# Optimization experiments

Measured on AMD Instinct MI355X. Metric: run time of the kernel, lower is better.

Reference implementation:

```python
import jax, jax.numpy as jnp
import numpy as np

EPS = 1e-8
EPS12 = 1e-12
TAU = 0.2
IOU_THRESHOLD = 0.5
NEG_INF = -1e9

N, C = 8192, 1024
HID, FGD, CLSD = 256, 64, 128


def setup_inputs() -> dict:
    key = jax.random.key(0)
    ks = jax.random.split(key, 16)
    roi_feats = jax.random.normal(ks[0], (N, C), dtype=jnp.float32)
    # labels in {-1 (ignore), 0 (bg), 1..20 (classes)}
    labels = jax.random.randint(ks[1], (N,), 0, 21, dtype=jnp.int64) - 1
    ious = jax.random.uniform(ks[2], (N,), dtype=jnp.float32)
    s = 0.02
    w1f = jax.random.normal(ks[3], (HID, C), dtype=jnp.float32) * s
    b1f = jnp.zeros((HID,), dtype=jnp.float32)
    w2f = jax.random.normal(ks[4], (FGD, HID), dtype=jnp.float32) * s
    b2f = jnp.zeros((FGD,), dtype=jnp.float32)
    w1c = jax.random.normal(ks[5], (HID, C), dtype=jnp.float32) * s
    b1c = jnp.zeros((HID,), dtype=jnp.float32)
    w2c = jax.random.normal(ks[6], (CLSD, HID), dtype=jnp.float32) * s
    b2c = jnp.zeros((CLSD,), dtype=jnp.float32)
    return {"roi_feats": roi_feats, "labels": labels, "ious": ious,
            "w1f": w1f, "b1f": b1f, "w2f": w2f, "b2f": b2f,
            "w1c": w1c, "b1c": b1c, "w2c": w2c, "b2c": b2c}


def _project_normalize(x, w1, b1, w2, b2):
    h = jax.nn.relu(x @ w1.T + b1)
    z = h @ w2.T + b2
    nrm = jnp.linalg.norm(z, axis=1, keepdims=True)  # F.normalize: z / max(||z||, eps)
    return z / jnp.maximum(nrm, EPS)


def _fg_bg_loss(z_fg, fg_mask, ignore_mask, iou_weight):
    n = z_fg.shape[0]
    anchor = fg_mask & ~ignore_mask
    eye = jnp.eye(n, dtype=bool)
    # pos_mask[i,j] = fg_mask[j] & ~ignore[j], self excluded
    pos = (fg_mask & ~ignore_mask)[None, :] & ~eye  # [N,N]
    sim = (z_fg @ z_fg.T) / TAU
    sim_exp = jnp.exp(sim) * (~eye).astype(sim.dtype)
    denom = sim_exp.sum(axis=1)  # [N]
    numer = jnp.sum(jnp.exp(sim) * pos.astype(sim.dtype), axis=1)  # [N]
    n_pos = pos.sum(axis=1)
    loss_i = -jnp.log((numer + EPS) / (denom + EPS))
    valid = anchor & (n_pos > 0)
    w = iou_weight
    num = jnp.sum(jnp.where(valid, loss_i * w, 0.0))
    den = jnp.sum(jnp.where(valid, w, 0.0)) + EPS
    return num / den


def _class_supcon_loss(z_cls, labels, fg_mask, ignore_mask, iou_weight):
    n = z_cls.shape[0]
    anchor = fg_mask & ~ignore_mask
    eye = jnp.eye(n, dtype=bool)
    valid_den = ~eye & ~ignore_mask[None, :]  # [N,N]
    # pos[i,j]: same label, j not ignored, labels[j] != 0, j != i, j valid
    pos = (labels[None, :] == labels[:, None]) & ~ignore_mask[None, :] & (labels[None, :] != 0)
    pos = pos & ~eye & valid_den
    sim = (z_cls @ z_cls.T) / TAU
    logits = jnp.where(valid_den, sim, NEG_INF)
    denom_log = jax.nn.logsumexp(logits, axis=1)  # [N]
    n_pos = pos.sum(axis=1)
    sum_pos = jnp.sum(jnp.where(pos, sim, 0.0), axis=1)
    n_pos_safe = jnp.maximum(n_pos, 1).astype(sim.dtype)
    loss_i = -(sum_pos - n_pos.astype(sim.dtype) * denom_log) / n_pos_safe
    valid = anchor & (n_pos > 0) & valid_den.any(axis=1)
    w = iou_weight
    num = jnp.sum(jnp.where(valid, loss_i * w, 0.0))
    den = jnp.sum(jnp.where(valid, w, 0.0)) + EPS12
    return num / den


def reference(roi_feats, labels, ious, w1f, b1f, w2f, b2f, w1c, b1c, w2c, b2c):
    z_fg = _project_normalize(roi_feats, w1f, b1f, w2f, b2f)
    z_cls = _project_normalize(roi_feats, w1c, b1c, w2c, b2c)
    ignore_mask = labels == -1
    bg_mask = (labels == 0) & ~ignore_mask
    fg_mask = (labels > 0) & ~ignore_mask
    iou_weight = jnp.where(ious > IOU_THRESHOLD, ious, 0.0)
    loss_fg_bg = _fg_bg_loss(z_fg, fg_mask, ignore_mask, iou_weight)
    loss_supcon = _class_supcon_loss(z_cls, labels, fg_mask, ignore_mask, iou_weight)
    # loss_weights = (1.0, 1.0); stacked as [loss_fg_bg, loss_supcon]
    return jnp.stack([loss_fg_bg * 1.0, loss_supcon * 1.0])
```

## Files before the change

### kernel.cpp

```cpp
#include <hip/hip_runtime.h>
#include <hip/hip_bf16.h>
#include <math.h>

#define N_ROI 8192
#define C_IN  1024
#define HIDD  256
#define FGD   64
#define CLSD  128
#define INV_TAU 5.0f
#define SCALE_LOG2E 7.2134752f
#define LN2F 0.69314718f

using frag_ab = __attribute__((ext_vector_type(8))) short;
using f32x16  = __attribute__((ext_vector_type(16))) float;

static __device__ __forceinline__ short f32_to_bf16_bits(float f) {
  unsigned u = __builtin_bit_cast(unsigned, f);
  u = (u + 0x7FFFu + ((u >> 16) & 1u)) >> 16;
  return (short)u;
}
static __device__ __forceinline__ float bf16_bits_to_f32(short b) {
  unsigned u = ((unsigned)(unsigned short)b) << 16;
  return __builtin_bit_cast(float, u);
}
static __device__ __forceinline__ float fast_exp2(float x) {
#if __has_builtin(__builtin_amdgcn_exp2f)
  return __builtin_amdgcn_exp2f(x);
#else
  return exp2f(x);
#endif
}
static __device__ __forceinline__ void async_copy16(const void* g, void* l) {
  __builtin_amdgcn_global_load_lds(
      (const __attribute__((address_space(1))) unsigned int*)g,
      (__attribute__((address_space(3))) unsigned int*)l, 16, 0, 0);
}

__global__ __launch_bounds__(256) void pack_zero_kernel(
    const float* __restrict__ w1f, const float* __restrict__ w1c,
    const float* __restrict__ w2f, const float* __restrict__ w2c,
    short* __restrict__ W1pf, short* __restrict__ W1pc,
    short* __restrict__ W2pf, short* __restrict__ W2pc,
    float* __restrict__ accum, int* __restrict__ cnt,
    float* __restrict__ Vc) {
  int b = blockIdx.x;
  if (b == 280) {
    int t = threadIdx.x;
    if (t < 8) accum[t] = 0.f;
    if (t < 24) cnt[t] = 0;
    for (int q = t; q < 2560; q += 256) Vc[q] = 0.f;
    return;
  }
  const float* src; short* dst; int Ksh; int b0;
  if (b < 128)      { src = w1f; dst = W1pf; Ksh = 10; b0 = 0; }
  else if (b < 256) { src = w1c; dst = W1pc; Ksh = 10; b0 = 128; }
  else if (b < 264) { src = w2f; dst = W2pf; Ksh = 8;  b0 = 256; }
  else              { src = w2c; dst = W2pc; Ksh = 8;  b0 = 264; }
  int K = 1 << Ksh;
  int f = (b - b0) * 256 + threadIdx.x;
  int r = f >> (Ksh - 3);
  int c0 = (f & ((K >> 3) - 1)) << 3;
  float4 v0 = *(const float4*)(src + (size_t)r * K + c0);
  float4 v1 = *(const float4*)(src + (size_t)r * K + c0 + 4);
  union { short s[8]; uint4 v; } o;
  o.s[0] = f32_to_bf16_bits(v0.x); o.s[1] = f32_to_bf16_bits(v0.y);
  o.s[2] = f32_to_bf16_bits(v0.z); o.s[3] = f32_to_bf16_bits(v0.w);
  o.s[4] = f32_to_bf16_bits(v1.x); o.s[5] = f32_to_bf16_bits(v1.y);
  o.s[6] = f32_to_bf16_bits(v1.z); o.s[7] = f32_to_bf16_bits(v1.w);
  ((uint4*)dst)[(size_t)((r >> 5) * (K >> 4) + (c0 >> 4)) * 64 +
                ((c0 >> 3) & 1) * 32 + (r & 31)] = o.v;
}

template<int D>
__device__ __forceinline__ void gemm2_from_lds(
    const short* __restrict__ T2,
    const short* __restrict__ W2p, const float* __restrict__ b2,
    short* __restrict__ Zr, float* __restrict__ tii,
    short* __restrict__ T, int gt) {
  int lane = threadIdx.x & 63;
  const frag_ab* Wv = (const frag_ab*)W2p;
  constexpr int NT = D / 32;
  frag_ab a[16];
  #pragma unroll
  for (int kc = 0; kc < 16; ++kc)
    a[kc] = *(const frag_ab*)&T2[(lane & 31) * 264 + kc * 16 + (lane >> 5) * 8];
  f32x16 acc[NT];
  #pragma unroll
  for (int j = 0; j < NT; ++j)
    #pragma unroll
    for (int q = 0; q < 16; ++q) acc[j][q] = 0.f;
  #pragma unroll
  for (int kc = 0; kc < 16; ++kc)
    #pragma unroll
    for (int j = 0; j < NT; ++j)
      acc[j] = __builtin_amdgcn_mfma_f32_32x32x16_bf16(a[kc], Wv[(j * 16 + kc) * 64 + lane], acc[j], 0, 0, 0);
  int c = lane & 31, h = lane >> 5;
  float bb[NT];
  #pragma unroll
  for (int j = 0; j < NT; ++j) bb[j] = b2[j * 32 + c];
  float s1[16];
  #pragma unroll
  for (int r = 0; r < 16; ++r) {
    s1[r] = 0.f;
    #pragma unroll
    for (int j = 0; j < NT; ++j) {
      float v = acc[j][r] + bb[j];
      s1[r] += v * v;
    }
  }
  #pragma unroll
  for (int r = 0; r < 16; ++r)
    #pragma unroll
    for (int m = 1; m < 32; m <<= 1) s1[r] += __shfl_xor(s1[r], m);
  float s2[16];
  #pragma unroll
  for (int r = 0; r < 16; ++r) s2[r] = 0.f;
  #pragma unroll
  for (int j = 0; j < NT; ++j) {
    int cl = j * 32 + c;
    #pragma unroll
    for (int g = 0; g < 4; ++g) {
      short q0, q1, q2, q3;
      #pragma unroll
      for (int e = 0; e < 4; ++e) {
        int r = g * 4 + e;
        float sc = 1.f / fmaxf(sqrtf(s1[r]), 1e-8f);
        short qb = f32_to_bf16_bits((acc[j][r] + bb[j]) * sc);
        float zf = bf16_bits_to_f32(qb);
        s2[r] += zf * zf;
        if (e == 0) q0 = qb; else if (e == 1) q1 = qb; else if (e == 2) q2 = qb; else q3 = qb;
      }
      *(short4*)&T[cl * 36 + 4 * h + 8 * g] = make_short4(q0, q1, q2, q3);
    }
  }
  #pragma unroll
  for (int r = 0; r < 16; ++r)
    #pragma unroll
    for (int m = 1; m < 32; m <<= 1) s2[r] += __shfl_xor(s2[r], m);
  if (c == 0) {
    #pragma unroll
    for (int r = 0; r < 16; ++r)
      tii[gt * 32 + (r & 3) + 8 * (r >> 2) + 4 * h] = s2[r];
  }
  uint4* Zv = (uint4*)Zr;
  #pragma unroll
  for (int k = 0; k < D / 16; ++k) {
    int c0 = (2 * k + h) * 8;
    union { short s[8]; uint4 u; } o;
    #pragma unroll
    for (int e = 0; e < 8; ++e) o.s[e] = T[(c0 + e) * 36 + c];
    Zv[(size_t)(gt * (D / 16) + k) * 64 + h * 32 + c] = o.u;
  }
}

__global__ __launch_bounds__(256) void fused_mlp_kernel(
    const float* __restrict__ X,
    const short* __restrict__ W1pf, const short* __restrict__ W1pc,
    const float* __restrict__ b1f, const float* __restrict__ b1c,
    const short* __restrict__ W2pf, const short* __restrict__ W2pc,
    const float* __restrict__ b2f, const float* __restrict__ b2c,
    short* __restrict__ Zrf, short* __restrict__ Zrc,
    float* __restrict__ tiif, float* __restrict__ tiic,
    const int* __restrict__ labels,
    float* __restrict__ Sfg, float* __restrict__ Pfg,
    float* __restrict__ Scls,
    float* __restrict__ pfv, float* __restrict__ nimv,
    int* __restrict__ cnt) {
  __shared__ short stageA[2][1024];
  __shared__ short T2[32 * 264];
  __shared__ short Tw[128 * 36];
  int tid = threadIdx.x, lane = tid & 63, wv = tid >> 6;
  int Mb = blockIdx.x, head = blockIdx.y;

  if (head == 0 && tid < 32) {
    int i = Mb * 32 + tid;
    Sfg[i] = 0.f; Pfg[i] = 0.f; Scls[i] = 0.f;
    int l = labels[i];
    pfv[i]  = (l > 0)  ? 1.f : 0.f;
    nimv[i] = (l != -1) ? 1.f : 0.f;
    int b = l + 1; if (b < 0) b = 0; if (b > 21) b = 21;
    atomicAdd(&cnt[b], 1);
  }

  const short* Wp = head ? W1pc : W1pf;
  const float* b1 = head ? b1c  : b1f;
  const uint4* Wv4 = (const uint4*)Wp;
  int arow = tid >> 3;
  int ac4  = tid & 7;
  const float* Xp = X + (size_t)(Mb * 32 + arow) * C_IN + ac4 * 4;
  int aslot = ((ac4 >> 2) * 64 + ((ac4 >> 1) & 1) * 32 + arow) * 8 + (ac4 & 1) * 4;

  float4 av[4];
  frag_ab breg[3][4];
  f32x16 acc[2];
  #pragma unroll
  for (int nt = 0; nt < 2; ++nt)
    #pragma unroll
    for (int q = 0; q < 16; ++q) acc[nt][q] = 0.f;

  auto loadA = [&](int c, int s) { av[s] = *(const float4*)(Xp + c * 32); };
  auto loadB = [&](int c, int s) {
    #pragma unroll
    for (int kci = 0; kci < 2; ++kci)
      #pragma unroll
      for (int nt = 0; nt < 2; ++nt)
        breg[s][kci * 2 + nt] =
            *(const frag_ab*)&Wv4[(size_t)((wv * 2 + nt) * 64 + c * 2 + kci) * 64 + lane];
  };
  auto storeA = [&](int buf, int s) {
    *(short4*)&stageA[buf][aslot] =
        make_short4(f32_to_bf16_bits(av[s].x), f32_to_bf16_bits(av[s].y),
                    f32_to_bf16_bits(av[s].z), f32_to_bf16_bits(av[s].w));
  };
  auto domfma = [&](int buf, int bank) {
    frag_ab a0 = *(const frag_ab*)&stageA[buf][(0 * 64 + lane) * 8];
    frag_ab a1 = *(const frag_ab*)&stageA[buf][(1 * 64 + lane) * 8];
    #pragma unroll
    for (int nt = 0; nt < 2; ++nt)
      acc[nt] = __builtin_amdgcn_mfma_f32_32x32x16_bf16(a0, breg[bank][nt], acc[nt], 0, 0, 0);
    #pragma unroll
    for (int nt = 0; nt < 2; ++nt)
      acc[nt] = __builtin_amdgcn_mfma_f32_32x32x16_bf16(a1, breg[bank][2 + nt], acc[nt], 0, 0, 0);
  };
  auto lds_barrier = [&]() {
    asm volatile("s_waitcnt lgkmcnt(0)" ::: "memory");
    __builtin_amdgcn_s_barrier();
    __builtin_amdgcn_sched_barrier(0);
  };

  loadA(0, 0); loadA(1, 1); loadA(2, 2); loadA(3, 3);
  loadB(0, 0); loadB(1, 1);
  storeA(0, 0);
  lds_barrier();

  #pragma unroll
  for (int c = 0; c < 32; ++c) {
    if (c + 2 < 32) loadB(c + 2, (c + 2) % 3);
    if (c + 4 < 32) loadA(c + 4, (c + 4) & 3);
    domfma(c & 1, c % 3);
    if (c + 1 < 32) {
      storeA((c + 1) & 1, (c + 1) & 3);
      lds_barrier();
    }
  }
  {
    int cl31 = lane & 31, h = lane >> 5;
    #pragma unroll
    for (int nt = 0; nt < 2; ++nt) {
      int gc = wv * 64 + nt * 32 + cl31;
      float bb = b1[gc];
      #pragma unroll
      for (int q = 0; q < 16; ++q) {
        int row = (q & 3) + 8 * (q >> 2) + 4 * h;
        float x = fmaxf(acc[nt][q] + bb, 0.f);
        T2[row * 264 + gc] = f32_to_bf16_bits(x);
      }
    }
  }
  __syncthreads();

  if (wv == 0) {
    if (head == 0)
      gemm2_from_lds<FGD>(T2, W2pf, b2f, Zrf, tiif, Tw, Mb);
    else
      gemm2_from_lds<CLSD>(T2, W2pc, b2c, Zrc, tiic, Tw, Mb);
  }
}

__global__ __launch_bounds__(128) void classsum_kernel(
    const short* __restrict__ Zrc, const int* __restrict__ labels,
    float* __restrict__ Vc) {
  __shared__ int lidx[512];
  __shared__ int lcnt;
  int c = blockIdx.x + 1;
  int d = threadIdx.x;
  int j0 = blockIdx.y * 512;
  if (d == 0) lcnt = 0;
  __syncthreads();
  #pragma unroll
  for (int u = 0; u < 4; ++u) {
    int row = j0 + u * 128 + d;
    if (labels[row] == c) {
      int k = atomicAdd(&lcnt, 1);
      lidx[k] = row;
    }
  }
  __syncthreads();
  int n = lcnt;
  int kc = d >> 4, h = (d >> 3) & 1, e = d & 7;
  float acc = 0.f;
  for (int k = 0; k < n; ++k) {
    int row = lidx[k];
    int jt = row >> 5, r = row & 31;
    acc += bf16_bits_to_f32(
        Zrc[((size_t)((jt * 8 + kc) * 64 + h * 32 + r)) * 8 + e]);
  }
  atomicAdd(&Vc[(c - 1) * 128 + d], acc);
}

template<int D, int MODE, int NJT>
__device__ __forceinline__ void loss_body(
    const short* __restrict__ Zr,
    const float* __restrict__ maskv,
    float* __restrict__ Sg, float* __restrict__ Pg,
    short* __restrict__ smem) {
  constexpr int KC = D / 16;
  constexpr int JP = 2;
  constexpr int NIT = NJT / JP;
  constexpr int BUFQ = JP * KC * 512;
  constexpr int LD = BUFQ / 4096;
  int tid = threadIdx.x, lane = tid & 63, wv = tid >> 6;
  int itile = (blockIdx.x >> 1) * 8 + wv;
  int jt0 = blockIdx.y * NJT;
  int jlane = lane & 31;
  const frag_ab* Zrv = (const frag_ab*)Zr;

  frag_ab a[KC];
  #pragma unroll
  for (int kc = 0; kc < KC; ++kc) {
    frag_ab t = Zrv[(itile * KC + kc) * 64 + lane];
    #pragma unroll
    for (int e = 0; e < 8; ++e)
      t[e] = f32_to_bf16_bits(bf16_bits_to_f32(t[e]) * SCALE_LOG2E);
    a[kc] = t;
  }
  __builtin_amdgcn_sched_barrier(0);
  asm volatile("s_waitcnt vmcnt(0)" ::: "memory");
  __builtin_amdgcn_sched_barrier(0);

  short* b0 = smem;
  short* b1 = smem + BUFQ;
  short* b2 = smem + 2 * BUFQ;
  float* maskf = (float*)(smem + 3 * BUFQ);

  async_copy16(maskv + jt0 * 32 + (size_t)(tid & 127) * 4,
               maskf + (wv & 1) * 256);

  auto STAGE = [&](short* dst, int it) {
    const short* src = Zr + (size_t)(jt0 + it * JP) * KC * 512;
    #pragma unroll
    for (int u = 0; u < LD; ++u)
      async_copy16(src + (size_t)(u * 512 + tid) * 8, dst + u * 4096 + wv * 512);
  };

  STAGE(b0, 0); STAGE(b1, 1);

  float Ssum[16] = {}, Psum[16] = {};

  #pragma unroll 1
  for (int t = 0; t < NIT; ++t) {
    if (t < NIT - 1) {
      if constexpr (LD == 1) asm volatile("s_waitcnt vmcnt(1)" ::: "memory");
      else                   asm volatile("s_waitcnt vmcnt(2)" ::: "memory");
    } else {
      asm volatile("s_waitcnt vmcnt(0)" ::: "memory");
    }
    __builtin_amdgcn_s_barrier();
    __builtin_amdgcn_sched_barrier(0);
    if (t + 2 < NIT) STAGE(b2, t + 2);

    float m0 = maskf[t * 64 + jlane];
    float m1 = maskf[t * 64 + 32 + jlane];
    f32x16 acc0, acc1;
    #pragma unroll
    for (int q = 0; q < 16; ++q) { acc0[q] = 0.f; acc1[q] = 0.f; }
    #pragma unroll
    for (int kc = 0; kc < KC; ++kc) {
      frag_ab bb0 = *(const frag_ab*)&b0[(kc * 64 + lane) * 8];
      frag_ab bb1 = *(const frag_ab*)&b0[((KC + kc) * 64 + lane) * 8];
      acc0 = __builtin_amdgcn_mfma_f32_32x32x16_bf16(a[kc], bb0, acc0, 0, 0, 0);
      acc1 = __builtin_amdgcn_mfma_f32_32x32x16_bf16(a[kc], bb1, acc1, 0, 0, 0);
    }
    #pragma unroll
    for (int rr = 0; rr < 16; ++rr) {
      float e0 = fast_exp2(acc0[rr]);
      float e1 = fast_exp2(acc1[rr]);
      if (MODE == 0) {
        Ssum[rr] += e0 + e1;
        Psum[rr] = fmaf(m0, e0, fmaf(m1, e1, Psum[rr]));
      } else {
        Ssum[rr] = fmaf(m1, e1, fmaf(m0, e0, Ssum[rr]));
      }
    }
    short* tmp = b0; b0 = b1; b1 = b2; b2 = tmp;
  }

  #pragma unroll
  for (int r = 0; r < 16; ++r) {
    float s = Ssum[r], p = Psum[r];
    #pragma unroll
    for (int m = 1; m < 32; m <<= 1) {
      s += __shfl_xor(s, m);
      if (MODE == 0) p += __shfl_xor(p, m);
    }
    if ((lane & 31) == 0) {
      int row = (r & 3) + 8 * (r >> 2) + 4 * (lane >> 5);
      atomicAdd(&Sg[itile * 32 + row], s);
      if (MODE == 0) atomicAdd(&Pg[itile * 32 + row], p);
    }
  }
}

__global__ __launch_bounds__(512, 2) void loss_kernel(
    const short* __restrict__ Zrf, const short* __restrict__ Zrc,
    const float* __restrict__ pfv, const float* __restrict__ nimv,
    float* __restrict__ Sfg, float* __restrict__ Pfg,
    float* __restrict__ Scls) {
  __shared__ short smem[3 * 8192 + 1024];
  if ((blockIdx.x & 1) == 0)
    loss_body<FGD, 0, 16>(Zrf, pfv, Sfg, Pfg, smem);
  else
    loss_body<CLSD, 1, 16>(Zrc, nimv, Scls, nullptr, smem);
}

__global__ __launch_bounds__(256) void finalize_kernel(
    const float* __restrict__ Sfg, const float* __restrict__ Pfg,
    const float* __restrict__ Scls,
    const short* __restrict__ Zrc, const float* __restrict__ Vc,
    const float* __restrict__ tiif, const float* __restrict__ tiic,
    const int* __restrict__ labels, const float* __restrict__ ious,
    int* __restrict__ cnt, float* __restrict__ accum, float* __restrict__ out) {
  int i = blockIdx.x * 256 + threadIdx.x;
  int l = labels[i];
  float iv = ious[i];
  float w = (iv > 0.5f) ? iv : 0.f;
  int cntP = 0;
  #pragma unroll
  for (int b = 2; b <= 21; ++b) cntP += cnt[b];
  int cntNI = N_ROI - cnt[0];
  bool Pi = (l > 0);
  float numF = 0.f, denF = 0.f, numC = 0.f, denC = 0.f;
  float eF = __expf(INV_TAU * tiif[i]);
  float Sf = Sfg[i] - eF;
  float Pf = Pfg[i] - (Pi ? eF : 0.f);
  int nposF = cntP - (Pi ? 1 : 0);
  if (Pi && nposF > 0) {
    float lossF = logf((Sf + 1e-8f) / (Pf + 1e-8f));
    numF = lossF * w; denF = w;
  }
  float tC = INV_TAU * tiic[i];
  float eC = __expf(tC);
  float Sc = Scls[i] - ((l != -1) ? eC : 0.f);
  float SPdot = 0.f;
  if (Pi) {
    const float* V = Vc + (size_t)(l - 1) * 128;
    int jt = i >> 5, r = i & 31;
    #pragma unroll
    for (int kc = 0; kc < 8; ++kc)
      #pragma unroll
      for (int h = 0; h < 2; ++h) {
        frag_ab z = *(const frag_ab*)&Zrc[((size_t)((jt * 8 + kc) * 64 + h * 32 + r)) * 8];
        #pragma unroll
        for (int e = 0; e < 8; ++e)
          SPdot += bf16_bits_to_f32(z[e]) * V[kc * 16 + h * 8 + e];
      }
  }
  float SP = SPdot * INV_TAU - (Pi ? tC : 0.f);
  int nposC = Pi ? (cnt[l + 1] - 1) : 0;
  bool anyv = (cntNI - ((l != -1) ? 1 : 0)) > 0;
  if (Pi && nposC > 0 && anyv) {
    float lse = logf(Sc);
    float lossC = -(SP - (float)nposC * lse) / fmaxf((float)nposC, 1.f);
    numC = lossC * w; denC = w;
  }
  float v0 = numF, v1 = denF, v2 = numC, v3 = denC;
  #pragma unroll
  for (int m = 1; m < 64; m <<= 1) {
    v0 += __shfl_xor(v0, m); v1 += __shfl_xor(v1, m);
    v2 += __shfl_xor(v2, m); v3 += __shfl_xor(v3, m);
  }
  __shared__ float red[4][4];
  int lane = threadIdx.x & 63, wid = threadIdx.x >> 6;
  if (lane == 0) { red[wid][0]=v0; red[wid][1]=v1; red[wid][2]=v2; red[wid][3]=v3; }
  __syncthreads();
  if (threadIdx.x == 0) {
    float s0=0,s1=0,s2=0,s3=0;
    for (int q = 0; q < 4; ++q) { s0+=red[q][0]; s1+=red[q][1]; s2+=red[q][2]; s3+=red[q][3]; }
    atomicAdd(&accum[0], s0); atomicAdd(&accum[1], s1);
    atomicAdd(&accum[2], s2); atomicAdd(&accum[3], s3);
    __threadfence();
    int t = atomicAdd(&cnt[22], 1);
    if (t == 31) {
      __threadfence();
      out[0] = accum[0] / (accum[1] + 1e-8f);
      out[1] = accum[2] / (accum[3] + 1e-12f);
    }
  }
}

extern "C" void kernel_launch(void* const* d_in, const int* in_sizes, int n_in,
                              void* d_out, int out_size, void* d_ws, size_t ws_size,
                              hipStream_t stream) {
  const float* X    = (const float*)d_in[0];
  const int*  labels= (const int*)d_in[1];
  const float* ious = (const float*)d_in[2];
  const float* w1f  = (const float*)d_in[3];
  const float* b1f  = (const float*)d_in[4];
  const float* w2f  = (const float*)d_in[5];
  const float* b2f  = (const float*)d_in[6];
  const float* w1c  = (const float*)d_in[7];
  const float* b1c  = (const float*)d_in[8];
  const float* w2c  = (const float*)d_in[9];
  const float* b2c  = (const float*)d_in[10];
  float* out = (float*)d_out;

  char* w = (char*)d_ws;
  short* W1pf = (short*)w;            w += 524288;
  short* W1pc = (short*)w;            w += 524288;
  short* W2pf = (short*)w;            w += 32768;
  short* W2pc = (short*)w;            w += 65536;
  short* Zrf  = (short*)w;            w += 1048576;
  short* Zrc  = (short*)w;            w += 2097152;
  float* Sfg  = (float*)w;            w += 32768;
  float* Pfg  = (float*)w;            w += 32768;
  float* Scls = (float*)w;            w += 32768;
  float* SPc  = (float*)w;            w += 32768;
  float* tiif = (float*)w;            w += 32768;
  float* tiic = (float*)w;            w += 32768;
  float* pfv  = (float*)w;            w += 32768;
  float* nimv = (float*)w;            w += 32768;
  float* ljmv = (float*)w;            w += 32768;
  float* accum= (float*)w;            w += 32;
  int*   cnt  = (int*)w;              w += 96;
  float* Vc   = (float*)w;            w += 10240;
  (void)SPc; (void)ljmv;

  pack_zero_kernel<<<281, 256, 0, stream>>>(w1f, w1c, w2f, w2c,
                                            W1pf, W1pc, W2pf, W2pc, accum, cnt, Vc);

  fused_mlp_kernel<<<dim3(256, 2), 256, 0, stream>>>(X, W1pf, W1pc, b1f, b1c,
                                            W2pf, W2pc, b2f, b2c,
                                            Zrf, Zrc, tiif, tiic,
                                            labels, Sfg, Pfg, Scls,
                                            pfv, nimv, cnt);

  classsum_kernel<<<dim3(20, 16), 128, 0, stream>>>(Zrc, labels, Vc);

  loss_kernel<<<dim3(64, 16), 512, 0, stream>>>(Zrf, Zrc, pfv, nimv,
                                                Sfg, Pfg, Scls);

  finalize_kernel<<<N_ROI/256, 256, 0, stream>>>(Sfg, Pfg, Scls, Zrc, Vc,
                                                 tiif, tiic,
                                                 labels, ious, cnt, accum, out);
}
```

Baseline: 184.3 us.

## Pre-pack X to bf16 MFMA layout and stream it via async LDS loads

```diff
diff --git a/kernel.cpp b/kernel.cpp
--- a/kernel.cpp
+++ b/kernel.cpp
@@ -37,10 +37,12 @@
 }
 
 __global__ __launch_bounds__(256) void pack_zero_kernel(
+    const float* __restrict__ X,
     const float* __restrict__ w1f, const float* __restrict__ w1c,
     const float* __restrict__ w2f, const float* __restrict__ w2c,
     short* __restrict__ W1pf, short* __restrict__ W1pc,
     short* __restrict__ W2pf, short* __restrict__ W2pc,
+    short* __restrict__ Xp16,
     float* __restrict__ accum, int* __restrict__ cnt,
     float* __restrict__ Vc) {
   int b = blockIdx.x;
@@ -49,6 +51,25 @@
     if (t < 8) accum[t] = 0.f;
     if (t < 24) cnt[t] = 0;
     for (int q = t; q < 2560; q += 256) Vc[q] = 0.f;
+    return;
+  }
+  if (b >= 281) {
+    int b2 = b - 281;
+    int Mb = b2 >> 4, cpair = b2 & 15;
+    int tid = threadIdx.x;
+    int c = cpair * 2 + (tid >> 7);
+    int tt = tid & 127;
+    int lane = tt & 63, kh = tt >> 6;
+    int row = lane & 31, hi = lane >> 5;
+    const float* src = X + (size_t)(Mb * 32 + row) * C_IN + c * 32 + kh * 16 + hi * 8;
+    float4 v0 = *(const float4*)src;
+    float4 v1 = *(const float4*)(src + 4);
+    union { short s[8]; uint4 v; } o;
+    o.s[0] = f32_to_bf16_bits(v0.x); o.s[1] = f32_to_bf16_bits(v0.y);
+    o.s[2] = f32_to_bf16_bits(v0.z); o.s[3] = f32_to_bf16_bits(v0.w);
+    o.s[4] = f32_to_bf16_bits(v1.x); o.s[5] = f32_to_bf16_bits(v1.y);
+    o.s[6] = f32_to_bf16_bits(v1.z); o.s[7] = f32_to_bf16_bits(v1.w);
+    *(uint4*)&Xp16[((size_t)(Mb * 32 + c)) * 1024 + (size_t)tt * 8] = o.v;
     return;
   }
   const float* src; short* dst; int Ksh; int b0;
@@ -154,7 +175,7 @@
 }
 
 __global__ __launch_bounds__(256) void fused_mlp_kernel(
-    const float* __restrict__ X,
+    const short* __restrict__ Xp16,
     const short* __restrict__ W1pf, const short* __restrict__ W1pc,
     const float* __restrict__ b1f, const float* __restrict__ b1c,
     const short* __restrict__ W2pf, const short* __restrict__ W2pc,
@@ -166,7 +187,7 @@
     float* __restrict__ Scls,
     float* __restrict__ pfv, float* __restrict__ nimv,
     int* __restrict__ cnt) {
-  __shared__ short stageA[2][1024];
+  __shared__ short ringA[4 * 1024];
   __shared__ short T2[32 * 264];
   __shared__ short Tw[128 * 36];
   int tid = threadIdx.x, lane = tid & 63, wv = tid >> 6;
@@ -181,16 +202,15 @@
     int b = l + 1; if (b < 0) b = 0; if (b > 21) b = 21;
     atomicAdd(&cnt[b], 1);
   }
+  __builtin_amdgcn_sched_barrier(0);
+  asm volatile("s_waitcnt vmcnt(0)" ::: "memory");
+  __builtin_amdgcn_sched_barrier(0);
 
   const short* Wp = head ? W1pc : W1pf;
   const float* b1 = head ? b1c  : b1f;
   const uint4* Wv4 = (const uint4*)Wp;
-  int arow = tid >> 3;
-  int ac4  = tid & 7;
-  const float* Xp = X + (size_t)(Mb * 32 + arow) * C_IN + ac4 * 4;
-  int aslot = ((ac4 >> 2) * 64 + ((ac4 >> 1) & 1) * 32 + arow) * 8 + (ac4 & 1) * 4;
-
-  float4 av[4];
+  int t127 = tid & 127;
+
   frag_ab breg[3][4];
   f32x16 acc[2];
   #pragma unroll
@@ -198,7 +218,10 @@
     #pragma unroll
     for (int q = 0; q < 16; ++q) acc[nt][q] = 0.f;
 
-  auto loadA = [&](int c, int s) { av[s] = *(const float4*)(Xp + c * 32); };
+  auto stageA = [&](int c, int slot) {
+    const short* src = Xp16 + ((size_t)(Mb * 32 + c)) * 1024 + (size_t)t127 * 8;
+    async_copy16(src, &ringA[slot * 1024 + t127 * 8]);
+  };
   auto loadB = [&](int c, int s) {
     #pragma unroll
     for (int kci = 0; kci < 2; ++kci)
@@ -207,14 +230,9 @@
         breg[s][kci * 2 + nt] =
             *(const frag_ab*)&Wv4[(size_t)((wv * 2 + nt) * 64 + c * 2 + kci) * 64 + lane];
   };
-  auto storeA = [&](int buf, int s) {
-    *(short4*)&stageA[buf][aslot] =
-        make_short4(f32_to_bf16_bits(av[s].x), f32_to_bf16_bits(av[s].y),
-                    f32_to_bf16_bits(av[s].z), f32_to_bf16_bits(av[s].w));
-  };
-  auto domfma = [&](int buf, int bank) {
-    frag_ab a0 = *(const frag_ab*)&stageA[buf][(0 * 64 + lane) * 8];
-    frag_ab a1 = *(const frag_ab*)&stageA[buf][(1 * 64 + lane) * 8];
+  auto domfma = [&](int slot, int bank) {
+    frag_ab a0 = *(const frag_ab*)&ringA[slot * 1024 + (0 * 64 + lane) * 8];
+    frag_ab a1 = *(const frag_ab*)&ringA[slot * 1024 + (1 * 64 + lane) * 8];
     #pragma unroll
     for (int nt = 0; nt < 2; ++nt)
       acc[nt] = __builtin_amdgcn_mfma_f32_32x32x16_bf16(a0, breg[bank][nt], acc[nt], 0, 0, 0);
@@ -222,26 +240,19 @@
     for (int nt = 0; nt < 2; ++nt)
       acc[nt] = __builtin_amdgcn_mfma_f32_32x32x16_bf16(a1, breg[bank][2 + nt], acc[nt], 0, 0, 0);
   };
-  auto lds_barrier = [&]() {
-    asm volatile("s_waitcnt lgkmcnt(0)" ::: "memory");
+
+  stageA(0, 0); stageA(1, 1); loadB(0, 0); stageA(2, 2); loadB(1, 1);
+
+  #pragma unroll
+  for (int c = 0; c < 32; ++c) {
+    if (c < 30)       asm volatile("s_waitcnt vmcnt(5)" ::: "memory");
+    else if (c == 30) asm volatile("s_waitcnt vmcnt(4)" ::: "memory");
+    else              asm volatile("s_waitcnt vmcnt(0)" ::: "memory");
     __builtin_amdgcn_s_barrier();
     __builtin_amdgcn_sched_barrier(0);
-  };
-
-  loadA(0, 0); loadA(1, 1); loadA(2, 2); loadA(3, 3);
-  loadB(0, 0); loadB(1, 1);
-  storeA(0, 0);
-  lds_barrier();
-
-  #pragma unroll
-  for (int c = 0; c < 32; ++c) {
+    if (c + 3 < 32) stageA(c + 3, (c + 3) & 3);
     if (c + 2 < 32) loadB(c + 2, (c + 2) % 3);
-    if (c + 4 < 32) loadA(c + 4, (c + 4) & 3);
-    domfma(c & 1, c % 3);
-    if (c + 1 < 32) {
-      storeA((c + 1) & 1, (c + 1) & 3);
-      lds_barrier();
-    }
+    domfma(c & 3, c % 3);
   }
   {
     int cl31 = lane & 31, h = lane >> 5;
@@ -523,12 +534,14 @@
   float* accum= (float*)w;            w += 32;
   int*   cnt  = (int*)w;              w += 96;
   float* Vc   = (float*)w;            w += 10240;
+  short* Xp16 = (short*)w;            w += 16777216;
   (void)SPc; (void)ljmv;
 
-  pack_zero_kernel<<<281, 256, 0, stream>>>(w1f, w1c, w2f, w2c,
-                                            W1pf, W1pc, W2pf, W2pc, accum, cnt, Vc);
-
-  fused_mlp_kernel<<<dim3(256, 2), 256, 0, stream>>>(X, W1pf, W1pc, b1f, b1c,
+  pack_zero_kernel<<<281 + 4096, 256, 0, stream>>>(X, w1f, w1c, w2f, w2c,
+                                            W1pf, W1pc, W2pf, W2pc, Xp16,
+                                            accum, cnt, Vc);
+
+  fused_mlp_kernel<<<dim3(256, 2), 256, 0, stream>>>(Xp16, W1pf, W1pc, b1f, b1c,
                                             W2pf, W2pc, b2f, b2c,
                                             Zrf, Zrc, tiif, tiic,
                                             labels, Sfg, Pfg, Scls,
```

Result: slower. 189.0 us (+2.6%).
